# Optimization experiments

Measured on AMD Instinct MI355X. Metric: run time of the kernel, lower is better.

The kernel has to match this reference:

```python
import jax, jax.numpy as jnp
import numpy as np

N_CELL, N_NET, N_GCELL = 50000, 10000, 20000
E = 100000
D = 32   # hidden_node = hidden_net = hidden_hanna = out_node = out_net
DP = 16  # hidden_pin = hidden_edge feats


def setup_inputs() -> dict:
    key = jax.random.key(0)
    ks = jax.random.split(key, 21)
    f = jax.random.normal
    ri = lambda k, n: jax.random.randint(k, (E,), 0, n, dtype=jnp.int32)
    return {
        'node_feat': f(ks[0], (N_CELL, D), jnp.float32),
        'net_feat': f(ks[1], (N_NET, D), jnp.float32),
        'pin_feat': f(ks[2], (E, DP), jnp.float32),
        'hanna_feat': f(ks[3], (N_GCELL, D), jnp.float32),
        'edge_feat': f(ks[4], (E, DP), jnp.float32),
        'pins_src': ri(ks[5], N_CELL), 'pins_dst': ri(ks[6], N_NET),
        'pinned_src': ri(ks[7], N_NET), 'pinned_dst': ri(ks[8], N_CELL),
        'connect_src': ri(ks[9], N_GCELL), 'connect_dst': ri(ks[10], N_GCELL),
        'pt_src': ri(ks[11], N_CELL), 'pt_dst': ri(ks[12], N_GCELL),
        'pf_src': ri(ks[13], N_GCELL), 'pf_dst': ri(ks[14], N_CELL),
        'W_net': f(ks[15], (D, D)) * 0.1, 'b_net': jnp.zeros((D,), jnp.float32),
        'W_topo': f(ks[16], (DP, D * D)) * 0.1, 'b_topo': jnp.zeros((D * D,), jnp.float32),
        'W_pins': f(ks[17], (D, D)) * 0.1, 'b_pins': jnp.zeros((D,), jnp.float32),
        'W_connect': f(ks[18], (D, D)) * 0.1, 'b_connect': jnp.zeros((D,), jnp.float32),
        'W_pt': f(ks[19], (D, D)) * 0.1, 'b_pt': jnp.zeros((D,), jnp.float32),
        'b_pinned': jnp.zeros((D,), jnp.float32), 'b_pf': jnp.zeros((D,), jnp.float32),
    }


def _deg(idx, n):
    # clamped degree, as DGL clamps to min 1
    return jnp.maximum(jax.ops.segment_sum(jnp.ones_like(idx, jnp.float32), idx, n), 1.0)


def graph_conv(h_src, W, b, src, dst, n_src, n_dst):
    # DGL GraphConv with norm='both': D_out^{-1/2} gather -> sum -> D_in^{-1/2}, then W, b
    feat = (h_src * _deg(src, n_src)[:, None] ** -0.5) @ W
    agg = jax.ops.segment_sum(feat[src], dst, n_dst)
    return agg * _deg(dst, n_dst)[:, None] ** -0.5 + b


def nn_conv(h_src, efeat, W_topo, b_topo, bias, src, dst, n_dst):
    # DGL NNConv (aggregator='mean'): per-edge weight from edge_func, mean over in-edges
    d_in = h_src.shape[1]
    w = (efeat @ W_topo + b_topo).reshape(-1, d_in, bias.shape[0])  # (E, d_in, d_out)
    m = jnp.einsum('ei,eio->eo', h_src[src], w)
    return jax.ops.segment_sum(m, dst, n_dst) / _deg(dst, n_dst)[:, None] + bias


def reference(node_feat, net_feat, pin_feat, hanna_feat, edge_feat,
              pins_src, pins_dst, pinned_src, pinned_dst, connect_src, connect_dst,
              pt_src, pt_dst, pf_src, pf_dst,
              W_net, b_net, W_topo, b_topo, W_pins, b_pins,
              W_connect, b_connect, W_pt, b_pt, b_pinned, b_pf):
    # 'pins': cell -> net (GraphConv)
    h_net = graph_conv(node_feat, W_pins, b_pins, pins_src, pins_dst, N_CELL, N_NET)
    # 'pinned': net -> cell (NNConv) + 'point-from': gcell -> cell (NNConv); agg='sum'
    h_cell = (nn_conv(net_feat, pin_feat, W_topo, b_topo, b_pinned, pinned_src, pinned_dst, N_CELL)
              + nn_conv(hanna_feat, edge_feat, W_topo, b_topo, b_pf, pf_src, pf_dst, N_CELL))
    # 'connect': gcell -> gcell + 'point-to': cell -> gcell (GraphConvs); agg='sum'
    h_gcell = (graph_conv(hanna_feat, W_connect, b_connect, connect_src, connect_dst, N_GCELL, N_GCELL)
               + graph_conv(node_feat, W_pt, b_pt, pt_src, pt_dst, N_CELL, N_GCELL))
    return (h_cell, h_net + net_feat @ W_net + b_net, h_gcell)
```

## Files before the change

### kernel.cpp

```cpp
#include <hip/hip_runtime.h>

typedef unsigned short u16;
typedef unsigned int u32;

#define NC 50000
#define NN 10000
#define NG 20000
#define NE 100000
#define NSCAN 150016
#define NBLK 74


__device__ __forceinline__ float bflo(u32 a) { return __uint_as_float(a << 16); }
__device__ __forceinline__ float bfhi(u32 a) { return __uint_as_float(a & 0xFFFF0000u); }
__device__ __forceinline__ u16 fbf(float f) {
  u32 u = __float_as_uint(f);
  return (u16)((u + 0x7FFFu + ((u >> 16) & 1u)) >> 16);
}

__device__ __forceinline__ float nn_msg(int e, int s, const float* __restrict__ ef,
                                        const u16* __restrict__ T,
                                        const float* __restrict__ C, int o) {
  const float4* efp = reinterpret_cast<const float4*>(ef + (size_t)e * 16);
  float4 ea = efp[0], eb = efp[1], ec = efp[2], ed = efp[3];
  const uint4* tp = reinterpret_cast<const uint4*>(T + (size_t)s * 512 + o * 16);
  uint4 ta = tp[0], tb = tp[1];
  float m = C[(size_t)s * 32 + o];
  m += ea.x * bflo(ta.x) + ea.y * bfhi(ta.x) + ea.z * bflo(ta.y) + ea.w * bfhi(ta.y);
  m += eb.x * bflo(ta.z) + eb.y * bfhi(ta.z) + eb.z * bflo(ta.w) + eb.w * bfhi(ta.w);
  m += ec.x * bflo(tb.x) + ec.y * bfhi(tb.x) + ec.z * bflo(tb.y) + ec.w * bfhi(tb.y);
  m += ed.x * bflo(tb.z) + ed.y * bfhi(tb.z) + ed.z * bflo(tb.w) + ed.w * bfhi(tb.w);
  return m;
}

__global__ __launch_bounds__(512, 2) void k_front(
    const float* __restrict__ feat_net, const float* __restrict__ feat_han,
    const float* __restrict__ W_topo, const float* __restrict__ b_topo,
    u16* __restrict__ T_net, u16* __restrict__ T_han,
    float* __restrict__ C_net, float* __restrict__ C_han,
    const int* __restrict__ pins_src, const int* __restrict__ pins_dst,
    const int* __restrict__ pinned_dst, const int* __restrict__ pf_dst,
    const int* __restrict__ connect_src, const int* __restrict__ connect_dst,
    const int* __restrict__ pt_src, const int* __restrict__ pt_dst,
    int* __restrict__ hist, int* __restrict__ srccnt) {
  int b = blockIdx.x;
  int tid = threadIdx.x;
  if (b < 469) {
    __shared__ float hs[64][32];
    int nd0 = b * 64;
    {
      int idx = tid * 4;
      int nl = idx >> 5, i = idx & 31;
      int ng = nd0 + nl;
      int ngc = min(ng, 29999);
      const float* rp = (ngc < NN) ? feat_net + (size_t)ngc * 32
                                   : feat_han + (size_t)(ngc - NN) * 32;
      *reinterpret_cast<float4*>(&hs[nl][i]) =
          *reinterpret_cast<const float4*>(rp + i);
    }
    int jj = tid & 255;
    int j0 = jj * 2, j1 = j0 + 1;
    int p0 = j0 & 15, o0 = j0 >> 4;
    int p1 = j1 & 15, o1 = j1 >> 4;
    float w0[32], w1[32];
#pragma unroll
    for (int i = 0; i < 32; i++) {
      w0[i] = W_topo[p0 * 1024 + i * 32 + o0];
      w1[i] = W_topo[p1 * 1024 + i * 32 + o1];
    }
    __syncthreads();
    int g = tid >> 8;
#pragma unroll 4
    for (int n = 0; n < 32; n++) {
      int nl = g * 32 + n;
      float a0 = 0.f, a1 = 0.f;
#pragma unroll
      for (int i = 0; i < 32; i++) {
        float h = hs[nl][i];
        a0 += h * w0[i];
        a1 += h * w1[i];
      }
      int s = nd0 + nl;
      if (s < 30000) {
        u32 pk = (u32)fbf(a0) | ((u32)fbf(a1) << 16);
        u32* dst = (s < NN)
            ? reinterpret_cast<u32*>(T_net + (size_t)s * 512 + j0)
            : reinterpret_cast<u32*>(T_han + (size_t)(s - NN) * 512 + j0);
        *dst = pk;
      }
    }
    return;
  }
  if (b < 2344) {
    int t = (b - 469) * 512 + tid;
    int s2 = t >> 5, o = t & 31;
    bool han = s2 >= NN;
    const float* feat = han ? feat_han : feat_net;
    float* C = han ? C_han : C_net;
    int s = han ? s2 - NN : s2;
    float acc = 0.f;
#pragma unroll 8
    for (int i = 0; i < 32; i++)
      acc += feat[(size_t)s * 32 + i] * b_topo[i * 32 + o];
    C[(size_t)s * 32 + o] = acc;
    return;
  }
  int e = (b - 2344) * 512 + tid;
  if (e >= NE) return;
  atomicAdd(&hist[pins_dst[e]], 1);
  atomicAdd(&hist[10000 + connect_dst[e]], 1);
  atomicAdd(&hist[30000 + pt_dst[e]], 1);
  atomicAdd(&hist[50000 + pinned_dst[e]], 1);
  atomicAdd(&hist[100000 + pf_dst[e]], 1);
  atomicAdd(&srccnt[pins_src[e]], 1);
  atomicAdd(&srccnt[50000 + connect_src[e]], 1);
  atomicAdd(&srccnt[70000 + pt_src[e]], 1);
}

__global__ __launch_bounds__(256) void k_scan1(
    const int* __restrict__ cnt, int* __restrict__ bsum) {
  __shared__ int sm[256];
  int b = blockIdx.x, tid = threadIdx.x;
  int base = b * 2048 + tid * 8;
  int tot = 0;
#pragma unroll
  for (int j = 0; j < 8; j++) {
    int i = base + j;
    tot += (i < NSCAN) ? cnt[i] : 0;
  }
  sm[tid] = tot;
  __syncthreads();
  for (int off = 128; off > 0; off >>= 1) {
    if (tid < off) sm[tid] += sm[tid + off];
    __syncthreads();
  }
  if (tid == 0) bsum[b] = sm[0];
}

__global__ __launch_bounds__(256) void k_scan3(
    const int* __restrict__ cnt, const int* __restrict__ bsum,
    int* __restrict__ bases) {
  __shared__ int sm[256];
  __shared__ int carry;
  int b = blockIdx.x, tid = threadIdx.x;
  if (tid == 0) {
    int run = 0;
    for (int i = 0; i < b; i++) run += bsum[i];
    carry = run;
  }
  int base = b * 2048 + tid * 8;
  int v[8];
  int tot = 0;
#pragma unroll
  for (int j = 0; j < 8; j++) {
    int i = base + j;
    v[j] = (i < NSCAN) ? cnt[i] : 0;
    tot += v[j];
  }
  sm[tid] = tot;
  __syncthreads();
  for (int off = 1; off < 256; off <<= 1) {
    int add = (tid >= off) ? sm[tid - off] : 0;
    __syncthreads();
    sm[tid] += add;
    __syncthreads();
  }
  int excl = sm[tid] - tot + carry;
#pragma unroll
  for (int j = 0; j < 8; j++) {
    int i = base + j;
    if (i < NSCAN) bases[i] = excl;
    excl += v[j];
  }
}

__global__ __launch_bounds__(512) void k_fill(
    const int* __restrict__ pins_src, const int* __restrict__ pins_dst,
    const int* __restrict__ connect_src, const int* __restrict__ connect_dst,
    const int* __restrict__ pt_src, const int* __restrict__ pt_dst,
    const int* __restrict__ pinned_src, const int* __restrict__ pinned_dst,
    const int* __restrict__ pf_src, const int* __restrict__ pf_dst,
    const int* __restrict__ srccnt,
    const int* __restrict__ bases, int* __restrict__ cursor,
    int2* __restrict__ csr_gc, int2* __restrict__ csr_nn) {
  int t = blockIdx.x * 512 + threadIdx.x;
  if (t >= 5 * NE) return;
  int r = (t >= NE) + (t >= 2 * NE) + (t >= 3 * NE) + (t >= 4 * NE);
  int e = t - r * NE;
  const int* srcs = r == 0 ? pins_src : r == 1 ? connect_src
                   : r == 2 ? pt_src : r == 3 ? pinned_src : pf_src;
  const int* dsts = r == 0 ? pins_dst : r == 1 ? connect_dst
                   : r == 2 ? pt_dst : r == 3 ? pinned_dst : pf_dst;
  int off = r == 0 ? 0 : r == 1 ? 10000 : r == 2 ? 30000 : r == 3 ? 50000 : 100000;
  int s = srcs[e];
  int g = off + dsts[e];
  int pos = atomicAdd(&cursor[g], 1);
  int cpos = bases[g] + pos;
  if (r < 3) {
    int soff = r == 0 ? 0 : r == 1 ? 50000 : 70000;
    float w = rsqrtf(fmaxf((float)srccnt[soff + s], 1.f));
    csr_gc[cpos] = make_int2(s, __float_as_int(w));
  } else {
    csr_nn[cpos - 300000] = make_int2(e, s);
  }
}

__global__ __launch_bounds__(512) void k_gc_gather(
    const int* __restrict__ hist, const int* __restrict__ bases,
    const int2* __restrict__ csr_gc,
    const float* __restrict__ node_feat, const float* __restrict__ hanna_feat,
    float* __restrict__ S_net, float* __restrict__ S_conn, float* __restrict__ S_pt) {
  int t = blockIdx.x * 512 + threadIdx.x;
  int rr = t >> 5, o = t & 31;
  int rel = (rr >= 10000) + (rr >= 30000);
  const float* feat = (rel == 1) ? hanna_feat : node_feat;
  float* S = rel == 0 ? S_net + (size_t)rr * 32
           : rel == 1 ? S_conn + (size_t)(rr - 10000) * 32
                      : S_pt + (size_t)(rr - 30000) * 32;
  int base = bases[rr], deg = hist[rr];
  float acc = 0.f;
  int k = 0;
  for (; k + 1 < deg; k += 2) {
    int2 pa = csr_gc[base + k], pb = csr_gc[base + k + 1];
    acc += feat[(size_t)pa.x * 32 + o] * __int_as_float(pa.y) +
           feat[(size_t)pb.x * 32 + o] * __int_as_float(pb.y);
  }
  if (k < deg) {
    int2 pa = csr_gc[base + k];
    acc += feat[(size_t)pa.x * 32 + o] * __int_as_float(pa.y);
  }
  S[o] = acc;
}

__global__ __launch_bounds__(512) void k_tail(
    const int* __restrict__ hist, const int* __restrict__ bases,
    const int2* __restrict__ csr_nn,
    const float* __restrict__ pin_feat, const float* __restrict__ edge_feat,
    const u16* __restrict__ T_net, const u16* __restrict__ T_han,
    const float* __restrict__ C_net, const float* __restrict__ C_han,
    const float* __restrict__ b_pinned, const float* __restrict__ b_pf,
    const float* __restrict__ S_net, const float* __restrict__ net_feat,
    const float* __restrict__ W_pins, const float* __restrict__ b_pins,
    const float* __restrict__ W_net, const float* __restrict__ b_net,
    const float* __restrict__ S_conn, const float* __restrict__ S_pt,
    const float* __restrict__ W_connect, const float* __restrict__ b_connect,
    const float* __restrict__ W_pt, const float* __restrict__ b_pt,
    float* __restrict__ out) {
  __shared__ float Wa[1024], Wb[1024];
  int b = blockIdx.x;
  if (b < 3125) {
    int t = b * 512 + threadIdx.x;
    int d = t >> 5, o = t & 31;
    float a0 = 0.f, a1 = 0.f;
    {
      int g = 50000 + d;
      int base = bases[g] - 300000, deg = hist[g];
      int k = 0;
      for (; k + 1 < deg; k += 2) {
        int2 ea = csr_nn[base + k], eb = csr_nn[base + k + 1];
        a0 += nn_msg(ea.x, ea.y, pin_feat, T_net, C_net, o) +
              nn_msg(eb.x, eb.y, pin_feat, T_net, C_net, o);
      }
      if (k < deg) {
        int2 ea = csr_nn[base + k];
        a0 += nn_msg(ea.x, ea.y, pin_feat, T_net, C_net, o);
      }
      a0 /= fmaxf((float)deg, 1.f);
    }
    {
      int g = 100000 + d;
      int base = bases[g] - 300000, deg = hist[g];
      int k = 0;
      for (; k + 1 < deg; k += 2) {
        int2 ea = csr_nn[base + k], eb = csr_nn[base + k + 1];
        a1 += nn_msg(ea.x, ea.y, edge_feat, T_han, C_han, o) +
              nn_msg(eb.x, eb.y, edge_feat, T_han, C_han, o);
      }
      if (k < deg) {
        int2 ea = csr_nn[base + k];
        a1 += nn_msg(ea.x, ea.y, edge_feat, T_han, C_han, o);
      }
      a1 /= fmaxf((float)deg, 1.f);
    }
    out[(size_t)d * 32 + o] = a0 + a1 + b_pinned[o] + b_pf[o];
    return;
  }
  if (b < 3750) {
    for (int k = threadIdx.x; k < 1024; k += 512) {
      Wa[k] = W_pins[k];
      Wb[k] = W_net[k];
    }
    __syncthreads();
    int t = (b - 3125) * 512 + threadIdx.x;
    int r = t >> 5, o = t & 31;
    float a1 = 0.f, a2 = 0.f;
#pragma unroll 8
    for (int i = 0; i < 32; i++) {
      a1 += S_net[(size_t)r * 32 + i] * Wa[i * 32 + o];
      a2 += net_feat[(size_t)r * 32 + i] * Wb[i * 32 + o];
    }
    out[1600000 + t] = a1 * rsqrtf(fmaxf((float)hist[r], 1.f)) + b_pins[o] +
                       a2 + b_net[o];
    return;
  }
  for (int k = threadIdx.x; k < 1024; k += 512) {
    Wa[k] = W_connect[k];
    Wb[k] = W_pt[k];
  }
  __syncthreads();
  int t = (b - 3750) * 512 + threadIdx.x;
  int r = t >> 5, o = t & 31;
  float a1 = 0.f, a2 = 0.f;
#pragma unroll 8
  for (int i = 0; i < 32; i++) {
    a1 += S_conn[(size_t)r * 32 + i] * Wa[i * 32 + o];
    a2 += S_pt[(size_t)r * 32 + i] * Wb[i * 32 + o];
  }
  out[1920000 + t] = a1 * rsqrtf(fmaxf((float)hist[10000 + r], 1.f)) + b_connect[o] +
                     a2 * rsqrtf(fmaxf((float)hist[30000 + r], 1.f)) + b_pt[o];
}

extern "C" void kernel_launch(void* const* d_in, const int* in_sizes, int n_in,
                              void* d_out, int out_size, void* d_ws, size_t ws_size,
                              hipStream_t stream) {
  const float* node_feat  = (const float*)d_in[0];
  const float* net_feat   = (const float*)d_in[1];
  const float* pin_feat   = (const float*)d_in[2];
  const float* hanna_feat = (const float*)d_in[3];
  const float* edge_feat  = (const float*)d_in[4];
  const int* pins_src    = (const int*)d_in[5];
  const int* pins_dst    = (const int*)d_in[6];
  const int* pinned_src  = (const int*)d_in[7];
  const int* pinned_dst  = (const int*)d_in[8];
  const int* connect_src = (const int*)d_in[9];
  const int* connect_dst = (const int*)d_in[10];
  const int* pt_src      = (const int*)d_in[11];
  const int* pt_dst      = (const int*)d_in[12];
  const int* pf_src      = (const int*)d_in[13];
  const int* pf_dst      = (const int*)d_in[14];
  const float* W_net     = (const float*)d_in[15];
  const float* b_net     = (const float*)d_in[16];
  const float* W_topo    = (const float*)d_in[17];
  const float* b_topo    = (const float*)d_in[18];
  const float* W_pins    = (const float*)d_in[19];
  const float* b_pins    = (const float*)d_in[20];
  const float* W_connect = (const float*)d_in[21];
  const float* b_connect = (const float*)d_in[22];
  const float* W_pt      = (const float*)d_in[23];
  const float* b_pt      = (const float*)d_in[24];
  const float* b_pinned  = (const float*)d_in[25];
  const float* b_pf      = (const float*)d_in[26];
  float* out = (float*)d_out;

  int* wi = (int*)d_ws;
  int* hist    = wi + 0;
  int* cursor  = wi + 150016;
  int* srccnt  = wi + 300032;
  int* bases   = wi + 420032;
  int* bsum    = wi + 570064;
  int2* csr_gc = (int2*)(wi + 570192);
  int2* csr_nn = (int2*)(wi + 1170192);
  float* wf = (float*)d_ws;
  float* S_net  = wf + 1570192;
  float* S_conn = wf + 1890192;
  float* S_pt   = wf + 2530192;
  float* C_net  = wf + 3170192;
  float* C_han  = wf + 3490192;
  u16* T_net = (u16*)((char*)d_ws + 16520832);
  u16* T_han = (u16*)((char*)d_ws + 16520832 + 10240000);

  hipMemsetAsync(d_ws, 0, 420032 * sizeof(int), stream);

  k_front<<<2540, 512, 0, stream>>>(
      net_feat, hanna_feat, W_topo, b_topo, T_net, T_han, C_net, C_han,
      pins_src, pins_dst, pinned_dst, pf_dst, connect_src, connect_dst,
      pt_src, pt_dst, hist, srccnt);

  k_scan1<<<NBLK, 256, 0, stream>>>(hist, bsum);
  k_scan3<<<NBLK, 256, 0, stream>>>(hist, bsum, bases);

  k_fill<<<(5 * NE + 511) / 512, 512, 0, stream>>>(
      pins_src, pins_dst, connect_src, connect_dst, pt_src, pt_dst,
      pinned_src, pinned_dst, pf_src, pf_dst, srccnt, bases, cursor,
      csr_gc, csr_nn);

  k_gc_gather<<<3125, 512, 0, stream>>>(
      hist, bases, csr_gc, node_feat, hanna_feat, S_net, S_conn, S_pt);

  k_tail<<<5000, 512, 0, stream>>>(
      hist, bases, csr_nn, pin_feat, edge_feat,
      T_net, T_han, C_net, C_han, b_pinned, b_pf,
      S_net, net_feat, W_pins, b_pins, W_net, b_net,
      S_conn, S_pt, W_connect, b_connect, W_pt, b_pt, out);
}
```

Measured before the change: 281.0 us.

## Co-schedule GraphConv and NNConv gathers in one interleaved kernel, vectorize topo matmul

After: 309.1 us. +10.0%, slower.

```diff
diff --git a/kernel.cpp b/kernel.cpp
--- a/kernel.cpp
+++ b/kernel.cpp
@@ -68,17 +68,24 @@
       w0[i] = W_topo[p0 * 1024 + i * 32 + o0];
       w1[i] = W_topo[p1 * 1024 + i * 32 + o1];
     }
+#pragma unroll
+    for (int i = 0; i < 32; i++) {
+      asm volatile("" : "+v"(w0[i]), "+v"(w1[i]));
+    }
     __syncthreads();
     int g = tid >> 8;
-#pragma unroll 4
+#pragma unroll 2
     for (int n = 0; n < 32; n++) {
       int nl = g * 32 + n;
+      const float4* hp = reinterpret_cast<const float4*>(&hs[nl][0]);
       float a0 = 0.f, a1 = 0.f;
 #pragma unroll
-      for (int i = 0; i < 32; i++) {
-        float h = hs[nl][i];
-        a0 += h * w0[i];
-        a1 += h * w1[i];
+      for (int q = 0; q < 8; q++) {
+        float4 h4 = hp[q];
+        a0 += h4.x * w0[4 * q] + h4.y * w0[4 * q + 1] +
+              h4.z * w0[4 * q + 2] + h4.w * w0[4 * q + 3];
+        a1 += h4.x * w1[4 * q] + h4.y * w1[4 * q + 1] +
+              h4.z * w1[4 * q + 2] + h4.w * w1[4 * q + 3];
       }
       int s = nd0 + nl;
       if (s < 30000) {
@@ -205,40 +212,78 @@
   }
 }
 
-__global__ __launch_bounds__(512) void k_gc_gather(
+__global__ __launch_bounds__(512) void k_gather(
     const int* __restrict__ hist, const int* __restrict__ bases,
-    const int2* __restrict__ csr_gc,
+    const int2* __restrict__ csr_gc, const int2* __restrict__ csr_nn,
     const float* __restrict__ node_feat, const float* __restrict__ hanna_feat,
-    float* __restrict__ S_net, float* __restrict__ S_conn, float* __restrict__ S_pt) {
-  int t = blockIdx.x * 512 + threadIdx.x;
-  int rr = t >> 5, o = t & 31;
-  int rel = (rr >= 10000) + (rr >= 30000);
-  const float* feat = (rel == 1) ? hanna_feat : node_feat;
-  float* S = rel == 0 ? S_net + (size_t)rr * 32
-           : rel == 1 ? S_conn + (size_t)(rr - 10000) * 32
-                      : S_pt + (size_t)(rr - 30000) * 32;
-  int base = bases[rr], deg = hist[rr];
-  float acc = 0.f;
-  int k = 0;
-  for (; k + 1 < deg; k += 2) {
-    int2 pa = csr_gc[base + k], pb = csr_gc[base + k + 1];
-    acc += feat[(size_t)pa.x * 32 + o] * __int_as_float(pa.y) +
-           feat[(size_t)pb.x * 32 + o] * __int_as_float(pb.y);
-  }
-  if (k < deg) {
-    int2 pa = csr_gc[base + k];
-    acc += feat[(size_t)pa.x * 32 + o] * __int_as_float(pa.y);
-  }
-  S[o] = acc;
-}
-
-__global__ __launch_bounds__(512) void k_tail(
-    const int* __restrict__ hist, const int* __restrict__ bases,
-    const int2* __restrict__ csr_nn,
     const float* __restrict__ pin_feat, const float* __restrict__ edge_feat,
     const u16* __restrict__ T_net, const u16* __restrict__ T_han,
     const float* __restrict__ C_net, const float* __restrict__ C_han,
     const float* __restrict__ b_pinned, const float* __restrict__ b_pf,
+    float* __restrict__ S_net, float* __restrict__ S_conn, float* __restrict__ S_pt,
+    float* __restrict__ out) {
+  int b = blockIdx.x;
+  if ((b & 1) == 0) {
+    int t = (b >> 1) * 512 + threadIdx.x;
+    int rr = t >> 5, o = t & 31;
+    int rel = (rr >= 10000) + (rr >= 30000);
+    const float* feat = (rel == 1) ? hanna_feat : node_feat;
+    float* S = rel == 0 ? S_net + (size_t)rr * 32
+             : rel == 1 ? S_conn + (size_t)(rr - 10000) * 32
+                        : S_pt + (size_t)(rr - 30000) * 32;
+    int base = bases[rr], deg = hist[rr];
+    float acc = 0.f;
+    int k = 0;
+    for (; k + 1 < deg; k += 2) {
+      int2 pa = csr_gc[base + k], pb = csr_gc[base + k + 1];
+      acc += feat[(size_t)pa.x * 32 + o] * __int_as_float(pa.y) +
+             feat[(size_t)pb.x * 32 + o] * __int_as_float(pb.y);
+    }
+    if (k < deg) {
+      int2 pa = csr_gc[base + k];
+      acc += feat[(size_t)pa.x * 32 + o] * __int_as_float(pa.y);
+    }
+    S[o] = acc;
+    return;
+  }
+  int t = (b >> 1) * 512 + threadIdx.x;
+  int d = t >> 5, o = t & 31;
+  float a0 = 0.f, a1 = 0.f;
+  {
+    int g = 50000 + d;
+    int base = bases[g] - 300000, deg = hist[g];
+    int k = 0;
+    for (; k + 1 < deg; k += 2) {
+      int2 ea = csr_nn[base + k], eb = csr_nn[base + k + 1];
+      a0 += nn_msg(ea.x, ea.y, pin_feat, T_net, C_net, o) +
+            nn_msg(eb.x, eb.y, pin_feat, T_net, C_net, o);
+    }
+    if (k < deg) {
+      int2 ea = csr_nn[base + k];
+      a0 += nn_msg(ea.x, ea.y, pin_feat, T_net, C_net, o);
+    }
+    a0 /= fmaxf((float)deg, 1.f);
+  }
+  {
+    int g = 100000 + d;
+    int base = bases[g] - 300000, deg = hist[g];
+    int k = 0;
+    for (; k + 1 < deg; k += 2) {
+      int2 ea = csr_nn[base + k], eb = csr_nn[base + k + 1];
+      a1 += nn_msg(ea.x, ea.y, edge_feat, T_han, C_han, o) +
+            nn_msg(eb.x, eb.y, edge_feat, T_han, C_han, o);
+    }
+    if (k < deg) {
+      int2 ea = csr_nn[base + k];
+      a1 += nn_msg(ea.x, ea.y, edge_feat, T_han, C_han, o);
+    }
+    a1 /= fmaxf((float)deg, 1.f);
+  }
+  out[(size_t)d * 32 + o] = a0 + a1 + b_pinned[o] + b_pf[o];
+}
+
+__global__ __launch_bounds__(512) void k_fin(
+    const int* __restrict__ hist,
     const float* __restrict__ S_net, const float* __restrict__ net_feat,
     const float* __restrict__ W_pins, const float* __restrict__ b_pins,
     const float* __restrict__ W_net, const float* __restrict__ b_net,
@@ -248,50 +293,13 @@
     float* __restrict__ out) {
   __shared__ float Wa[1024], Wb[1024];
   int b = blockIdx.x;
-  if (b < 3125) {
-    int t = b * 512 + threadIdx.x;
-    int d = t >> 5, o = t & 31;
-    float a0 = 0.f, a1 = 0.f;
-    {
-      int g = 50000 + d;
-      int base = bases[g] - 300000, deg = hist[g];
-      int k = 0;
-      for (; k + 1 < deg; k += 2) {
-        int2 ea = csr_nn[base + k], eb = csr_nn[base + k + 1];
-        a0 += nn_msg(ea.x, ea.y, pin_feat, T_net, C_net, o) +
-              nn_msg(eb.x, eb.y, pin_feat, T_net, C_net, o);
-      }
-      if (k < deg) {
-        int2 ea = csr_nn[base + k];
-        a0 += nn_msg(ea.x, ea.y, pin_feat, T_net, C_net, o);
-      }
-      a0 /= fmaxf((float)deg, 1.f);
-    }
-    {
-      int g = 100000 + d;
-      int base = bases[g] - 300000, deg = hist[g];
-      int k = 0;
-      for (; k + 1 < deg; k += 2) {
-        int2 ea = csr_nn[base + k], eb = csr_nn[base + k + 1];
-        a1 += nn_msg(ea.x, ea.y, edge_feat, T_han, C_han, o) +
-              nn_msg(eb.x, eb.y, edge_feat, T_han, C_han, o);
-      }
-      if (k < deg) {
-        int2 ea = csr_nn[base + k];
-        a1 += nn_msg(ea.x, ea.y, edge_feat, T_han, C_han, o);
-      }
-      a1 /= fmaxf((float)deg, 1.f);
-    }
-    out[(size_t)d * 32 + o] = a0 + a1 + b_pinned[o] + b_pf[o];
-    return;
-  }
-  if (b < 3750) {
+  if (b < 625) {
     for (int k = threadIdx.x; k < 1024; k += 512) {
       Wa[k] = W_pins[k];
       Wb[k] = W_net[k];
     }
     __syncthreads();
-    int t = (b - 3125) * 512 + threadIdx.x;
+    int t = b * 512 + threadIdx.x;
     int r = t >> 5, o = t & 31;
     float a1 = 0.f, a2 = 0.f;
 #pragma unroll 8
@@ -308,7 +316,7 @@
     Wb[k] = W_pt[k];
   }
   __syncthreads();
-  int t = (b - 3750) * 512 + threadIdx.x;
+  int t = (b - 625) * 512 + threadIdx.x;
   int r = t >> 5, o = t & 31;
   float a1 = 0.f, a2 = 0.f;
 #pragma unroll 8
@@ -384,12 +392,12 @@
       pinned_src, pinned_dst, pf_src, pf_dst, srccnt, bases, cursor,
       csr_gc, csr_nn);
 
-  k_gc_gather<<<3125, 512, 0, stream>>>(
-      hist, bases, csr_gc, node_feat, hanna_feat, S_net, S_conn, S_pt);
-
-  k_tail<<<5000, 512, 0, stream>>>(
-      hist, bases, csr_nn, pin_feat, edge_feat,
-      T_net, T_han, C_net, C_han, b_pinned, b_pf,
-      S_net, net_feat, W_pins, b_pins, W_net, b_net,
+  k_gather<<<6250, 512, 0, stream>>>(
+      hist, bases, csr_gc, csr_nn, node_feat, hanna_feat,
+      pin_feat, edge_feat, T_net, T_han, C_net, C_han, b_pinned, b_pf,
+      S_net, S_conn, S_pt, out);
+
+  k_fin<<<1875, 512, 0, stream>>>(
+      hist, S_net, net_feat, W_pins, b_pins, W_net, b_net,
       S_conn, S_pt, W_connect, b_connect, W_pt, b_pt, out);
 }
```
